# Optimization experiments

Measured on AMD Instinct MI355X. Metric: run time of the kernel, lower is better.

Reference implementation:

```python
import jax, jax.numpy as jnp
import numpy as np

B, T, HID = 2, 2048, 2048
NH, NKV, HD = 32, 8, 64


def setup_inputs() -> dict:
    key = jax.random.key(0)
    ks = jax.random.split(key, 5)
    x = jax.random.normal(ks[0], (B, T, HID), dtype=jnp.float32)
    position_ids = jnp.broadcast_to(jnp.arange(T, dtype=jnp.int32), (B, T))
    s = 0.02
    Wq = jax.random.normal(ks[1], (NH * HD, HID), dtype=jnp.float32) * s
    Wk = jax.random.normal(ks[2], (NKV * HD, HID), dtype=jnp.float32) * s
    Wv = jax.random.normal(ks[3], (NKV * HD, HID), dtype=jnp.float32) * s
    Wo = jax.random.normal(ks[4], (HID, NH * HD), dtype=jnp.float32) * s
    return {"x": x, "position_ids": position_ids, "Wq": Wq, "Wk": Wk, "Wv": Wv, "Wo": Wo}


def _rotate_half(t):
    t1, t2 = jnp.split(t, 2, axis=-1)
    return jnp.concatenate([-t2, t1], axis=-1)


def reference(x, position_ids, Wq, Wk, Wv, Wo):
    Bd, Td, _ = x.shape
    q = (x @ Wq.T).reshape(Bd, Td, NH, HD)
    k = (x @ Wk.T).reshape(Bd, Td, NKV, HD)
    v = (x @ Wv.T).reshape(Bd, Td, NKV, HD)

    # DummyRotaryEmbedding: freqs over even indices, repeat_interleave(2)
    freqs = 1.0 / (10000.0 ** (jnp.arange(0, HD, 2, dtype=jnp.float32) / HD))
    angles = position_ids.astype(jnp.float32)[:, :, None] * freqs  # [B,T,HD/2]
    cos = jnp.repeat(jnp.cos(angles), 2, axis=-1)[:, :, None, :]   # [B,T,1,HD]
    sin = jnp.repeat(jnp.sin(angles), 2, axis=-1)[:, :, None, :]

    q = q * cos + _rotate_half(q) * sin
    k = k * cos + _rotate_half(k) * sin

    n_rep = NH // NKV
    k = jnp.repeat(k, n_rep, axis=2)  # [B,T,NH,HD]
    v = jnp.repeat(v, n_rep, axis=2)

    scale = 1.0 / np.sqrt(HD).astype(np.float32)
    scores = jnp.einsum('bqhd,bkhd->bhqk', q, k) * scale  # [B,NH,T,T]
    probs = jax.nn.softmax(scores, axis=-1)
    out = jnp.einsum('bhqk,bkhd->bqhd', probs, v).reshape(Bd, Td, NH * HD)
    return out @ Wo.T
```

## Files before the change

kernel.cpp:

```cpp
#include <hip/hip_runtime.h>
#include <hip/hip_bf16.h>
#include <stdint.h>


typedef __attribute__((ext_vector_type(8))) short short8;
typedef __attribute__((ext_vector_type(4))) float f32x4;
typedef __attribute__((ext_vector_type(16))) float f32x16;

__device__ __forceinline__ unsigned short f2bf(float f) {
  union { float f; uint32_t u; } x; x.f = f;
  uint32_t r = x.u + 0x7fffu + ((x.u >> 16) & 1u);
  return (unsigned short)(r >> 16);
}
__device__ __forceinline__ float bf2f(unsigned short u) {
  union { uint32_t u; float f; } x; x.u = ((uint32_t)u) << 16;
  return x.f;
}
__device__ __forceinline__ uint32_t cvt_pk_bf16(float a, float b) {
  uint32_t r;
  asm("v_cvt_pk_bf16_f32 %0, %1, %2" : "=v"(r) : "v"(a), "v"(b));
  return r;
}
__device__ __forceinline__ void pl32swap(uint32_t& dst, uint32_t& src) {
  asm("v_permlane32_swap_b32 %0, %1" : "+v"(dst), "+v"(src));
}

__device__ __forceinline__ void gload_lds16(const void* g, void* l) {
  __builtin_amdgcn_global_load_lds(
      (const __attribute__((address_space(1))) unsigned int*)g,
      (__attribute__((address_space(3))) unsigned int*)l, 16, 0, 0);
}

#define VMCNT(n) asm volatile("s_waitcnt vmcnt(" #n ")" ::: "memory")
#define LGKMCNT0 asm volatile("s_waitcnt lgkmcnt(0)" ::: "memory")

__global__ __launch_bounds__(256) void convert_kernel(
    const float* __restrict__ x, const float* __restrict__ Wq,
    const float* __restrict__ Wk, const float* __restrict__ Wv,
    const float* __restrict__ Wo,
    unsigned short* __restrict__ xb, unsigned short* __restrict__ wqkvb,
    unsigned short* __restrict__ wob) {
  const int NX = 1048576;
  const int NQ = 524288;
  const int NK = 131072;
  const int NV = 131072;
  const int NO = 524288;
  const int total = NX + NQ + NK + NV + NO;
  for (int i = blockIdx.x * blockDim.x + threadIdx.x; i < total;
       i += gridDim.x * blockDim.x) {
    const float4* s; unsigned short* d; int o;
    if (i < NX)                 { o = i;               s = (const float4*)x;  d = xb; }
    else if (i < NX+NQ)         { o = i-NX;            s = (const float4*)Wq; d = wqkvb; }
    else if (i < NX+NQ+NK)      { o = i-NX-NQ;         s = (const float4*)Wk; d = wqkvb + 4194304; }
    else if (i < NX+NQ+NK+NV)   { o = i-NX-NQ-NK;      s = (const float4*)Wv; d = wqkvb + 5242880; }
    else                        { o = i-NX-NQ-NK-NV;   s = (const float4*)Wo; d = wob; }
    float4 v0 = s[(size_t)o * 2];
    float4 v1 = s[(size_t)o * 2 + 1];
    short8 r;
    r[0] = (short)f2bf(v0.x); r[1] = (short)f2bf(v0.y);
    r[2] = (short)f2bf(v0.z); r[3] = (short)f2bf(v0.w);
    r[4] = (short)f2bf(v1.x); r[5] = (short)f2bf(v1.y);
    r[6] = (short)f2bf(v1.z); r[7] = (short)f2bf(v1.w);
    *(short8*)(d + (size_t)o * 8) = r;
  }
}

template <int NQ, typename OutT>
__global__ __launch_bounds__(512, 2) void gemm_2cu(
    const unsigned short* __restrict__ A, const unsigned short* __restrict__ Bt,
    OutT* __restrict__ C, int N, int K) {
  __shared__ unsigned short lA[2][128 * 64];
  __shared__ unsigned short lB[2][NQ * 64 * 64];
  const int tid  = threadIdx.x;
  const int lane = tid & 63;
  const int w    = tid >> 6;
  const int wr   = w >> 2, wc = w & 3;
  const long tm  = (long)blockIdx.y * 128;
  const long tn  = (long)blockIdx.x * (NQ * 64);

  f32x4 acc[4][NQ];
#pragma unroll
  for (int fi = 0; fi < 4; ++fi)
#pragma unroll
    for (int nq = 0; nq < NQ; ++nq) acc[fi][nq] = (f32x4){0.f, 0.f, 0.f, 0.f};

  const int srow = tid >> 3;
  const int sgr  = ((tid & 7) ^ (srow & 7)) * 8;
  const unsigned short* ga = A  + (tm + srow) * (long)K + sgr;
  const unsigned short* gb = Bt + (tn + srow) * (long)K + sgr;

  int aoff[4][2], boff[NQ][2];
#pragma unroll
  for (int fi = 0; fi < 4; ++fi)
#pragma unroll
    for (int ks = 0; ks < 2; ++ks) {
      int gk = (lane >> 4) + ks * 4;
      aoff[fi][ks] = (wr * 64 + fi * 16 + (lane & 15)) * 128 + ((gk ^ (lane & 7)) << 4);
    }
#pragma unroll
  for (int nq = 0; nq < NQ; ++nq)
#pragma unroll
    for (int ks = 0; ks < 2; ++ks) {
      int gk = (lane >> 4) + ks * 4;
      boff[nq][ks] = (wc * (NQ * 16) + nq * 16 + (lane & 15)) * 128 + ((gk ^ (lane & 7)) << 4);
    }

#pragma unroll
  for (int i = 0; i < 2; ++i)  gload_lds16(ga + (long)(64 * i) * K, &lA[0][tid * 8 + 4096 * i]);
#pragma unroll
  for (int i = 0; i < NQ; ++i) gload_lds16(gb + (long)(64 * i) * K, &lB[0][tid * 8 + 4096 * i]);
  VMCNT(0);
  __builtin_amdgcn_s_barrier();

  const int nk = K >> 6;
  for (int t = 0; t < nk; ++t) {
    const int slot = t & 1;
    const unsigned short* gaT = ga + (long)((t + 1) << 6);
    const unsigned short* gbT = gb + (long)((t + 1) << 6);
    const bool st = (t + 1 < nk);
    const char* As = (const char*)lA[slot];
    const char* Bs = (const char*)lB[slot];
    unsigned short* dA = &lA[slot ^ 1][tid * 8];
    unsigned short* dB = &lB[slot ^ 1][tid * 8];

    short8 af[4][2];
#pragma unroll
    for (int nq = 0; nq < NQ; ++nq) {
      if (nq == 0) {
#pragma unroll
        for (int fi = 0; fi < 4; ++fi)
#pragma unroll
          for (int ks = 0; ks < 2; ++ks)
            af[fi][ks] = *(const short8*)(As + aoff[fi][ks]);
      }
      short8 bf0 = *(const short8*)(Bs + boff[nq][0]);
      short8 bf1 = *(const short8*)(Bs + boff[nq][1]);
      if (st && nq == 0) {
        gload_lds16(gaT,                 dA);
        gload_lds16(gaT + (long)64 * K,  dA + 4096);
#pragma unroll
        for (int i = 0; i < NQ; ++i)
          gload_lds16(gbT + (long)(64 * i) * K, dB + 4096 * i);
      }
      __builtin_amdgcn_s_barrier();
      LGKMCNT0;
      __builtin_amdgcn_sched_barrier(0);
      __builtin_amdgcn_s_setprio(1);
#pragma unroll
      for (int fi = 0; fi < 4; ++fi)
        acc[fi][nq] = __builtin_amdgcn_mfma_f32_16x16x32_bf16(af[fi][0], bf0, acc[fi][nq], 0, 0, 0);
#pragma unroll
      for (int fi = 0; fi < 4; ++fi)
        acc[fi][nq] = __builtin_amdgcn_mfma_f32_16x16x32_bf16(af[fi][1], bf1, acc[fi][nq], 0, 0, 0);
      __builtin_amdgcn_s_setprio(0);
      __builtin_amdgcn_sched_barrier(0);
      if (nq == NQ - 1) VMCNT(0);
      __builtin_amdgcn_s_barrier();
    }
  }

#pragma unroll
  for (int fi = 0; fi < 4; ++fi)
#pragma unroll
    for (int nq = 0; nq < NQ; ++nq) {
      long col = tn + wc * (NQ * 16) + nq * 16 + (lane & 15);
#pragma unroll
      for (int i = 0; i < 4; ++i) {
        long row = tm + wr * 64 + fi * 16 + (lane >> 4) * 4 + i;
        float v = acc[fi][nq][i];
        if constexpr (sizeof(OutT) == 2) C[row * N + col] = (OutT)f2bf(v);
        else                             C[row * N + col] = (OutT)v;
      }
    }
}

__global__ __launch_bounds__(256) void rope_kernel(
    unsigned short* __restrict__ qkv, const int* __restrict__ pos_ids) {
  const int m = blockIdx.x;
  const int tid = threadIdx.x;
  const float QSCALE = 0.18033688011112042f;
  __shared__ float cs[32], sn[32];
  if (tid < 32) {
    float pos = (float)pos_ids[m];
    float a = pos * exp2f(-(float)tid * 0.4152410118609203f);
    float s_, c_;
    sincosf(a, &s_, &c_);
    cs[tid] = c_; sn[tid] = s_;
  }
  __syncthreads();
  unsigned short* row = qkv + (size_t)m * 3072;

  const int qc = tid * 8;
  short8 qa = *(const short8*)(row + qc);
  short8 qp = *(const short8*)(row + (qc ^ 32));
  short8 ka = {}, kp = {};
  if (tid < 64) {
    const int kc = 2048 + tid * 8;
    ka = *(const short8*)(row + kc);
    kp = *(const short8*)(row + (kc ^ 32));
  }
  __syncthreads();

  {
    const int dbase = qc & 63;
    const float sgn = (qc & 32) ? 1.0f : -1.0f;
    short8 out;
#pragma unroll
    for (int j = 0; j < 8; ++j) {
      int fi = (dbase + j) >> 1;
      float o = bf2f((unsigned short)qa[j]) * cs[fi] +
                sgn * bf2f((unsigned short)qp[j]) * sn[fi];
      out[j] = (short)f2bf(o * QSCALE);
    }
    *(short8*)(row + qc) = out;
  }
  if (tid < 64) {
    const int kc = 2048 + tid * 8;
    const int dbase = (tid * 8) & 63;
    const float sgn = ((tid * 8) & 32) ? 1.0f : -1.0f;
    short8 out;
#pragma unroll
    for (int j = 0; j < 8; ++j) {
      int fi = (dbase + j) >> 1;
      float o = bf2f((unsigned short)ka[j]) * cs[fi] +
                sgn * bf2f((unsigned short)kp[j]) * sn[fi];
      out[j] = (short)f2bf(o);
    }
    *(short8*)(row + kc) = out;
  }
}

__global__ __launch_bounds__(256) void vtrans_kernel(
    const unsigned short* __restrict__ qkv, unsigned short* __restrict__ Vt) {
  const int tb = blockIdx.x, g = blockIdx.y, b = blockIdx.z;
  const int tid = threadIdx.x;
  __shared__ unsigned short lt[64 * 72];

  {
    const int r = tid >> 2, c = (tid & 3) * 16;
    const unsigned short* src =
        qkv + ((size_t)(b * 2048 + tb * 64 + r)) * 3072 + 2560 + g * 64 + c;
    short8 v0 = *(const short8*)(src);
    short8 v1 = *(const short8*)(src + 8);
    *(short8*)&lt[r * 72 + c] = v0;
    *(short8*)&lt[r * 72 + c + 8] = v1;
  }
  __syncthreads();

  {
    const int d = tid >> 2, t0 = (tid & 3) * 16;
    short8 o0, o1;
#pragma unroll
    for (int j = 0; j < 8; ++j) o0[j] = (short)lt[(t0 + j) * 72 + d];
#pragma unroll
    for (int j = 0; j < 8; ++j) o1[j] = (short)lt[(t0 + 8 + j) * 72 + d];
    unsigned short* dst =
        Vt + ((size_t)((b * 8 + g) * 64 + d)) * 2048 + tb * 64 + t0;
    *(short8*)(dst) = o0;
    *(short8*)(dst + 8) = o1;
  }
}

__global__ __launch_bounds__(512) void attn_kernel(
    const unsigned short* __restrict__ qkv,
    const unsigned short* __restrict__ Vt,
    unsigned short* __restrict__ attnout) {
  const int qt = blockIdx.x, g = blockIdx.y, b = blockIdx.z;
  const int tid = threadIdx.x, lane = tid & 63, w = tid >> 6;
  const int l31 = lane & 31, hi = lane >> 5;
  const int h = g * 4 + (w & 3);
  const int qbase = qt * 64 + (w >> 2) * 32;

  __shared__ unsigned short lK[2][64 * 64];
  __shared__ unsigned short lV[3][64 * 64];

  short8 qf[4];
  {
    const unsigned short* qrow =
        qkv + ((size_t)(b * 2048 + qbase + l31)) * 3072 + h * 64 + hi * 8;
#pragma unroll
    for (int kc = 0; kc < 4; ++kc) qf[kc] = *(const short8*)(qrow + kc * 16);
  }

  f32x16 o0, o1;
#pragma unroll
  for (int i = 0; i < 16; ++i) { o0[i] = 0.f; o1[i] = 0.f; }
  float lrun = 0.f;

  const unsigned short* kgbase = qkv + (size_t)b * 2048 * 3072 + 2048 + g * 64;
  const unsigned short* vgbase = Vt + ((size_t)(b * 8 + g) * 64) * 2048;
  const int srow = w * 8 + (lane >> 3);
  const int sg = ((lane & 7) ^ (srow & 7)) * 8;

  int koff[2][4];
#pragma unroll
  for (int s = 0; s < 2; ++s)
#pragma unroll
    for (int kc = 0; kc < 4; ++kc) {
      int r = s * 32 + l31;
      koff[s][kc] = r * 128 + (((kc * 2 + hi) ^ (r & 7)) << 4);
    }

#define STAGE(kbuf, vbuf, kb)                                                       \
  {                                                                                 \
    const unsigned short* kk_ = kgbase + (size_t)((kb) * 64) * 3072;                \
    const unsigned short* vv_ = vgbase + (kb) * 64;                                 \
    gload_lds16(kk_ + (size_t)srow * 3072 + sg, &lK[kbuf][(w * 8) * 64]);           \
    gload_lds16(vv_ + (size_t)srow * 2048 + sg, &lV[vbuf][(w * 8) * 64]);           \
  }

#define PV_BLOCK(VBASE)                                                             \
  {                                                                                 \
    const char* Vb_ = (VBASE);                                                      \
    _Pragma("unroll")                                                               \
    for (int ks = 0; ks < 2; ++ks) {                                                \
      union { uint32_t u[4]; short8 s8; } fa, fb;                                   \
      _Pragma("unroll")                                                             \
      for (int u = 0; u < 4; ++u) { fa.u[u] = wd[ks][u]; fb.u[u] = wd[ks][4 + u]; } \
      const int kk0 = ks * 2, kk1 = ks * 2 + 1;                                     \
      short8 va0 = *(const short8*)(Vb_ + koff[0][kk0]);                            \
      short8 va1 = *(const short8*)(Vb_ + koff[1][kk0]);                            \
      o0 = __builtin_amdgcn_mfma_f32_32x32x16_bf16(fa.s8, va0, o0, 0, 0, 0);        \
      o1 = __builtin_amdgcn_mfma_f32_32x32x16_bf16(fa.s8, va1, o1, 0, 0, 0);        \
      short8 vb0 = *(const short8*)(Vb_ + koff[0][kk1]);                            \
      short8 vb1 = *(const short8*)(Vb_ + koff[1][kk1]);                            \
      o0 = __builtin_amdgcn_mfma_f32_32x32x16_bf16(fb.s8, vb0, o0, 0, 0, 0);        \
      o1 = __builtin_amdgcn_mfma_f32_32x32x16_bf16(fb.s8, vb1, o1, 0, 0, 0);        \
    }                                                                               \
  }

  uint32_t wd[2][8];

  STAGE(0, 0, 0);
  __syncthreads();

  int vnext = 1;
#pragma unroll 1
  for (int t = 0; t < 32; ++t) {
    if (t + 1 < 32) STAGE((t + 1) & 1, vnext, t + 1);
    const char* Kb = (const char*)lK[t & 1];
    const int vprev = (vnext == 2) ? 0 : vnext + 1;

    f32x16 s0, s1;
#pragma unroll
    for (int i = 0; i < 16; ++i) { s0[i] = 0.f; s1[i] = 0.f; }
    __builtin_amdgcn_s_setprio(1);
#pragma unroll
    for (int kc = 0; kc < 4; ++kc) {
      short8 k0 = *(const short8*)(Kb + koff[0][kc]);
      short8 k1 = *(const short8*)(Kb + koff[1][kc]);
      s0 = __builtin_amdgcn_mfma_f32_32x32x16_bf16(k0, qf[kc], s0, 0, 0, 0);
      s1 = __builtin_amdgcn_mfma_f32_32x32x16_bf16(k1, qf[kc], s1, 0, 0, 0);
    }
    if (t > 0) PV_BLOCK((const char*)lV[vprev]);
    __builtin_amdgcn_s_setprio(0);

#pragma unroll
    for (int i = 0; i < 16; ++i) { s0[i] = __builtin_amdgcn_exp2f(s0[i]); lrun += s0[i]; }
#pragma unroll
    for (int i = 0; i < 16; ++i) { s1[i] = __builtin_amdgcn_exp2f(s1[i]); lrun += s1[i]; }

#pragma unroll
    for (int mi = 0; mi < 8; ++mi) {
      wd[0][mi] = cvt_pk_bf16(s0[2 * mi], s0[2 * mi + 1]);
      wd[1][mi] = cvt_pk_bf16(s1[2 * mi], s1[2 * mi + 1]);
    }
#pragma unroll
    for (int ks = 0; ks < 2; ++ks) {
      pl32swap(wd[ks][0], wd[ks][2]);
      pl32swap(wd[ks][1], wd[ks][3]);
      pl32swap(wd[ks][4], wd[ks][6]);
      pl32swap(wd[ks][5], wd[ks][7]);
    }

    vnext = (vnext == 2) ? 0 : vnext + 1;
    __syncthreads();
  }

  PV_BLOCK((const char*)lV[1]);

  lrun += __shfl_xor(lrun, 32);
  float inv = 1.0f / lrun;
  const size_t obase =
      (size_t)(b * 2048 + qbase) * 2048 + h * 64 + l31;
#pragma unroll
  for (int reg = 0; reg < 16; ++reg) {
    int q = (reg & 3) + 8 * (reg >> 2) + 4 * hi;
    float invq = __shfl(inv, q);
    attnout[obase + (size_t)q * 2048]      = f2bf(o0[reg] * invq);
    attnout[obase + (size_t)q * 2048 + 32] = f2bf(o1[reg] * invq);
  }
#undef STAGE
#undef PV_BLOCK
}

extern "C" void kernel_launch(void* const* d_in, const int* in_sizes, int n_in,
                              void* d_out, int out_size, void* d_ws, size_t ws_size,
                              hipStream_t stream) {
  (void)in_sizes; (void)n_in; (void)out_size; (void)ws_size;
  const float* x  = (const float*)d_in[0];
  const int* pos  = (const int*)d_in[1];
  const float* Wq = (const float*)d_in[2];
  const float* Wk = (const float*)d_in[3];
  const float* Wv = (const float*)d_in[4];
  const float* Wo = (const float*)d_in[5];
  float* out = (float*)d_out;
  char* ws = (char*)d_ws;

  unsigned short* xb      = (unsigned short*)(ws);
  unsigned short* wqkvb   = (unsigned short*)(ws + 16777216);
  unsigned short* wob     = (unsigned short*)(ws + 29360128);
  unsigned short* qkv     = (unsigned short*)(ws + 37748736);
  unsigned short* Vt      = (unsigned short*)(ws + 62914560);
  unsigned short* attnout = (unsigned short*)(ws + 67108864);

  convert_kernel<<<2048, 256, 0, stream>>>(x, Wq, Wk, Wv, Wo, xb, wqkvb, wob);
  gemm_2cu<3, unsigned short><<<dim3(16, 32), 512, 0, stream>>>(xb, wqkvb, qkv, 3072, 2048);
  rope_kernel<<<4096, 256, 0, stream>>>(qkv, pos);
  vtrans_kernel<<<dim3(32, 8, 2), 256, 0, stream>>>(qkv, Vt);
  attn_kernel<<<dim3(32, 8, 2), 512, 0, stream>>>(qkv, Vt, attnout);
  gemm_2cu<2, float><<<dim3(16, 32), 512, 0, stream>>>(attnout, wob, out, 2048, 2048);
}
```

Before: 196.4 us.

## Deepen K/V prefetch pipeline to two stages with vmcnt-based barriers

```diff
diff --git a/kernel.cpp b/kernel.cpp
--- a/kernel.cpp
+++ b/kernel.cpp
@@ -271,8 +271,8 @@
   const int h = g * 4 + (w & 3);
   const int qbase = qt * 64 + (w >> 2) * 32;
 
-  __shared__ unsigned short lK[2][64 * 64];
-  __shared__ unsigned short lV[3][64 * 64];
+  __shared__ unsigned short lK[3][64 * 64];
+  __shared__ unsigned short lV[4][64 * 64];
 
   short8 qf[4];
   {
@@ -282,9 +282,9 @@
     for (int kc = 0; kc < 4; ++kc) qf[kc] = *(const short8*)(qrow + kc * 16);
   }
 
-  f32x16 o0, o1;
-#pragma unroll
-  for (int i = 0; i < 16; ++i) { o0[i] = 0.f; o1[i] = 0.f; }
+  f32x16 o0, o1, zro;
+#pragma unroll
+  for (int i = 0; i < 16; ++i) { o0[i] = 0.f; o1[i] = 0.f; zro[i] = 0.f; }
   float lrun = 0.f;
 
   const unsigned short* kgbase = qkv + (size_t)b * 2048 * 3072 + 2048 + g * 64;
@@ -332,27 +332,34 @@
   uint32_t wd[2][8];
 
   STAGE(0, 0, 0);
-  __syncthreads();
-
-  int vnext = 1;
+  STAGE(1, 1, 1);
+  VMCNT(2);
+  __builtin_amdgcn_s_barrier();
+  __builtin_amdgcn_sched_barrier(0);
+
+  int kcur = 0;
+  int kst  = 2;
 #pragma unroll 1
   for (int t = 0; t < 32; ++t) {
-    if (t + 1 < 32) STAGE((t + 1) & 1, vnext, t + 1);
-    const char* Kb = (const char*)lK[t & 1];
-    const int vprev = (vnext == 2) ? 0 : vnext + 1;
+    if (t < 30) STAGE(kst, (t + 2) & 3, t + 2);
+    const char* Kb = (const char*)lK[kcur];
 
     f32x16 s0, s1;
-#pragma unroll
-    for (int i = 0; i < 16; ++i) { s0[i] = 0.f; s1[i] = 0.f; }
     __builtin_amdgcn_s_setprio(1);
-#pragma unroll
-    for (int kc = 0; kc < 4; ++kc) {
+    {
+      short8 k0 = *(const short8*)(Kb + koff[0][0]);
+      short8 k1 = *(const short8*)(Kb + koff[1][0]);
+      s0 = __builtin_amdgcn_mfma_f32_32x32x16_bf16(k0, qf[0], zro, 0, 0, 0);
+      s1 = __builtin_amdgcn_mfma_f32_32x32x16_bf16(k1, qf[0], zro, 0, 0, 0);
+    }
+#pragma unroll
+    for (int kc = 1; kc < 4; ++kc) {
       short8 k0 = *(const short8*)(Kb + koff[0][kc]);
       short8 k1 = *(const short8*)(Kb + koff[1][kc]);
       s0 = __builtin_amdgcn_mfma_f32_32x32x16_bf16(k0, qf[kc], s0, 0, 0, 0);
       s1 = __builtin_amdgcn_mfma_f32_32x32x16_bf16(k1, qf[kc], s1, 0, 0, 0);
     }
-    if (t > 0) PV_BLOCK((const char*)lV[vprev]);
+    if (t > 0) PV_BLOCK((const char*)lV[(t - 1) & 3]);
     __builtin_amdgcn_s_setprio(0);
 
 #pragma unroll
@@ -373,11 +380,15 @@
       pl32swap(wd[ks][5], wd[ks][7]);
     }
 
-    vnext = (vnext == 2) ? 0 : vnext + 1;
-    __syncthreads();
-  }
-
-  PV_BLOCK((const char*)lV[1]);
+    if (t < 30) { VMCNT(2); } else { VMCNT(0); }
+    __builtin_amdgcn_s_barrier();
+    __builtin_amdgcn_sched_barrier(0);
+
+    kcur = (kcur == 2) ? 0 : kcur + 1;
+    kst  = (kst == 2) ? 0 : kst + 1;
+  }
+
+  PV_BLOCK((const char*)lV[3]);
 
   lrun += __shfl_xor(lrun, 32);
   float inv = 1.0f / lrun;
```

Result: no change. 195.9 us (median of 2 runs) (-0.3%).
